# Optimization experiments

Measured on AMD Instinct MI355X. Metric: run time of the kernel, lower is better.

## Reference

```python
import jax, jax.numpy as jnp
import numpy as np
import math

# dims
B, T, D = 2, 1024, 1024
HQ, HKV, KD, VD = 16, 4, 64, 64   # query heads, kv heads, key dim, value dim
G = HQ // HKV                      # query group size
E, TOPK, CAP_FRAC, HID = 8, 2, 0.5, 2048
BASE = 10000.0
EPS = 1e-6


def setup_inputs() -> dict:
    key = jax.random.key(0)
    ks = jax.random.split(key, 12)
    s = jnp.float32(0.02)
    return {
        'x': jax.random.normal(ks[0], (B, T, D), jnp.float32),
        'wq': jax.random.normal(ks[1], (D, KD * HQ), jnp.float32) * s,
        'wk': jax.random.normal(ks[2], (D, KD * HKV), jnp.float32) * s,
        'wv': jax.random.normal(ks[3], (D, VD * HKV), jnp.float32) * s,
        'wo': jax.random.normal(ks[4], (G * HKV * VD, D), jnp.float32) * s,
        'router_w': jax.random.normal(ks[5], (D, E), jnp.float32) * s,
        'router_b': jax.random.normal(ks[6], (E,), jnp.float32) * s,
        'w1': jax.random.normal(ks[7], (E, D, HID), jnp.float32) * s,
        'w2': jax.random.normal(ks[8], (E, D, HID), jnp.float32) * s,
        'w3': jax.random.normal(ks[9], (E, HID, D), jnp.float32) * s,
        'norm1_scale': jnp.ones((D,), jnp.float32),
        'norm2_scale': jnp.ones((D,), jnp.float32),
    }


def _rms(x, scale):
    return x * jax.lax.rsqrt(jnp.mean(x * x, axis=-1, keepdims=True) + EPS) * scale


def _rope(x):
    # x: (B, t, H, d); rotary per RotaryEmbedding: tile(ticks,(1,2)), neg-half rotation
    t, d = x.shape[1], x.shape[3]
    thetas = BASE ** (-jnp.arange(0, d, 2, dtype=jnp.float32) / d)
    ticks = jnp.outer(jnp.arange(t, dtype=jnp.float32), thetas)
    ticks = jnp.tile(ticks, (1, 2))[None, :, None, :]
    cos, sin = jnp.cos(ticks).astype(x.dtype), jnp.sin(ticks).astype(x.dtype)
    x1, x2 = jnp.split(x, 2, axis=-1)
    neg = jnp.concatenate([-x2, x1], axis=-1)
    return x * cos + neg * sin


def reference(x, wq, wk, wv, wo, router_w, router_b, w1, w2, w3, norm1_scale, norm2_scale):
    b, t, d = x.shape
    # ---- pre-norm grouped-query attention with rotary, causal ----
    h = _rms(x, norm1_scale)
    q = (h @ wq).reshape(b, t, HQ, KD)
    k = (h @ wk).reshape(b, t, HKV, KD)
    v = (h @ wv).reshape(b, t, HKV, VD)
    q = _rope(q)
    k = _rope(k)
    qg = q.reshape(b, t, HKV, G, KD)
    scores = jnp.einsum('bthgk,bshk->bhgts', qg, k) / jnp.sqrt(jnp.asarray(KD, x.dtype))
    causal = jnp.tril(jnp.ones((t, t), bool))
    scores = jnp.where(causal, scores, jnp.asarray(-1e9, scores.dtype))
    probs = jax.nn.softmax(scores, axis=-1)
    attn = jnp.einsum('bhgts,bshv->bthgv', probs, v).reshape(b, t, HQ * VD)
    x = x + attn @ wo
    # ---- pre-norm top-k MoE feed-forward (capacity-masked dispatch/combine) ----
    h2 = _rms(x, norm2_scale)
    xf = h2.reshape(b * t, d)
    logits = xf.astype(jnp.float32) @ router_w + router_b        # router in fp32
    gate, assign = jax.lax.top_k(logits, TOPK)                   # (N,k)
    gate = jax.nn.softmax(gate, axis=-1).astype(x.dtype)
    cap = math.floor(b * t * CAP_FRAC)
    onehot = jax.nn.one_hot(assign, E, dtype=jnp.float32)        # (N,k,E)
    pos = jnp.cumsum(jnp.cumsum(onehot, axis=0), axis=1).astype(jnp.int32)
    mask = onehot * (pos < cap)                                  # capacity mask
    token_mask = jnp.sum(mask, axis=-1)                          # (N,k)
    choices = jnp.sum(jax.nn.one_hot(pos, cap, dtype=jnp.float32) * mask[..., None], axis=1)  # (N,E,cap)
    choices = choices.transpose(1, 2, 0)                         # (E,cap,N)
    exp_idx = jnp.einsum('tke,e->tk', mask, jnp.arange(E, dtype=jnp.float32)).astype(jnp.int32)
    pos_idx = jnp.einsum('tke,tke->tk', mask, pos.astype(jnp.float32)).astype(jnp.int32)
    grouped = jnp.einsum('ect,tD->ecD', choices.astype(x.dtype), xf)  # dispatch: (E,cap,D)
    # gated FF per expert: act(w2(x) * w1(x)) @ w3
    hh = jax.nn.gelu(jnp.einsum('ecd,edh->ech', grouped, w2) * jnp.einsum('ecd,edh->ech', grouped, w1))
    eout = jnp.einsum('ech,ehd->ecd', hh, w3)                    # (E,cap,D)
    gathered = eout[exp_idx, pos_idx].reshape(b, t, TOPK, d)
    tm = token_mask.reshape(b, t, TOPK)
    moe = jnp.where(tm[..., None] != 0, gathered, h2[:, :, None, :])  # dropped tokens fall back to input
    moe = jnp.einsum('btkD,btk->btD', moe, gate.reshape(b, t, TOPK))
    return x + moe
```

## Files before the change

### kernel.cpp

```cpp
#include <hip/hip_runtime.h>
#include <math.h>

#define Dm 1024
#define Tn 1024
#define Bn 2
#define NTOK 2048
#define HQn 16
#define HKVn 4
#define KDn 64
#define VDn 64
#define Gn 4
#define NE 8
#define CAPn 1024
#define HIDn 2048
#define QKVS 1536

using frag_ab = __attribute__((ext_vector_type(8))) short;
using f32x4  = __attribute__((ext_vector_type(4))) float;

__device__ __forceinline__ unsigned short f2bf(float f) {
    union { float f; unsigned int u; } v; v.f = f;
    unsigned int r = v.u + 0x7FFFu + ((v.u >> 16) & 1u);
    return (unsigned short)(r >> 16);
}
__device__ __forceinline__ float bf2f(unsigned short b) {
    union { unsigned int u; float f; } v; v.u = ((unsigned int)b) << 16;
    return v.f;
}
__device__ __forceinline__ float gelu_fast(float y) {
    float z = 0.7978845608028654f * (y + 0.044715f * y * y * y);
    float az = fabsf(z);
    float t = __expf(-2.f * az);
    float th = (1.f - t) / (1.f + t);
    th = copysignf(th, z);
    return 0.5f * y * (1.f + th);
}

#define GLOAD16(gp, lp) __builtin_amdgcn_global_load_lds( \
    (const __attribute__((address_space(1))) void*)(gp), \
    (__attribute__((address_space(3))) void*)(lp), 16, 0, 0)

#define LGKM_DRAIN() do { \
    asm volatile("s_waitcnt lgkmcnt(0)" ::: "memory"); \
    __builtin_amdgcn_sched_barrier(0); \
} while (0)

__global__ void rmsnorm_bf16_kernel(const float* __restrict__ x, const float* __restrict__ scale,
                                    unsigned short* __restrict__ out) {
    int row = blockIdx.x;
    const float* xr = x + (size_t)row * Dm;
    float ss = 0.f;
    for (int d = threadIdx.x; d < Dm; d += 256) { float v = xr[d]; ss += v * v; }
    __shared__ float red[256];
    red[threadIdx.x] = ss; __syncthreads();
    for (int s = 128; s > 0; s >>= 1) {
        if (threadIdx.x < s) red[threadIdx.x] += red[threadIdx.x + s];
        __syncthreads();
    }
    float inv = rsqrtf(red[0] * (1.f / Dm) + 1e-6f);
    for (int d = threadIdx.x; d < Dm; d += 256)
        out[(size_t)row * Dm + d] = f2bf(xr[d] * inv * scale[d]);
}

__global__ void rmsnorm_router_kernel(const float* __restrict__ x2, const float* __restrict__ scale,
                                      const float* __restrict__ rw, const float* __restrict__ rb,
                                      float* __restrict__ h2, int* __restrict__ assign,
                                      float* __restrict__ gate) {
    int row = blockIdx.x;
    const float* xr = x2 + (size_t)row * Dm;
    __shared__ float red[256];
    __shared__ float rowbuf[Dm];
    __shared__ float logits[NE];
    float v4[4]; float ss = 0.f;
    #pragma unroll
    for (int i = 0; i < 4; ++i) { v4[i] = xr[threadIdx.x + 256 * i]; ss += v4[i] * v4[i]; }
    red[threadIdx.x] = ss; __syncthreads();
    for (int s = 128; s > 0; s >>= 1) {
        if (threadIdx.x < s) red[threadIdx.x] += red[threadIdx.x + s];
        __syncthreads();
    }
    float inv = rsqrtf(red[0] * (1.f / Dm) + 1e-6f);
    #pragma unroll
    for (int i = 0; i < 4; ++i) {
        int d = threadIdx.x + 256 * i;
        float h = v4[i] * inv * scale[d];
        h2[(size_t)row * Dm + d] = h;
        rowbuf[d] = h;
    }
    __syncthreads();
    int e = threadIdx.x >> 5, lane32 = threadIdx.x & 31;
    float part = 0.f;
    for (int d = lane32; d < Dm; d += 32) part += rowbuf[d] * rw[(size_t)d * NE + e];
    for (int off = 16; off; off >>= 1) part += __shfl_down(part, off, 32);
    if (lane32 == 0) logits[e] = part + rb[e];
    __syncthreads();
    if (threadIdx.x == 0) {
        int i0 = 0; float m0 = logits[0];
        for (int i = 1; i < NE; ++i) if (logits[i] > m0) { m0 = logits[i]; i0 = i; }
        int i1 = -1; float m1 = -1e30f;
        for (int i = 0; i < NE; ++i) if (i != i0 && logits[i] > m1) { m1 = logits[i]; i1 = i; }
        float e1 = __expf(m1 - m0);
        float s = 1.f + e1;
        assign[row * 2] = i0; assign[row * 2 + 1] = i1;
        gate[row * 2] = 1.f / s; gate[row * 2 + 1] = e1 / s;
    }
}

__global__ void transpose_convert(const float* __restrict__ in, unsigned short* __restrict__ out,
                                  int R, int Cstride, int c_base) {
    int e = blockIdx.z;
    int Cext = gridDim.x * 64;
    in  += (size_t)e * R * Cstride;
    out += (size_t)e * R * Cext;
    __shared__ float T[64][65];
    int tid = threadIdx.x;
    int r0 = blockIdx.y * 64, c0 = blockIdx.x * 64;
    #pragma unroll
    for (int rep = 0; rep < 4; ++rep) {
        int r = (tid >> 4) + rep * 16;
        int c = (tid & 15) * 4;
        float4 v = *(const float4*)(in + (size_t)(r0 + r) * Cstride + c_base + c0 + c);
        T[r][c] = v.x; T[r][c + 1] = v.y; T[r][c + 2] = v.z; T[r][c + 3] = v.w;
    }
    __syncthreads();
    #pragma unroll
    for (int rep = 0; rep < 4; ++rep) {
        int c = rep * 16 + (tid >> 4);
        int r = (tid & 15) * 4;
        unsigned long long pk = (unsigned long long)f2bf(T[r][c])
                              | ((unsigned long long)f2bf(T[r + 1][c]) << 16)
                              | ((unsigned long long)f2bf(T[r + 2][c]) << 32)
                              | ((unsigned long long)f2bf(T[r + 3][c]) << 48);
        *(unsigned long long*)(out + (size_t)(c0 + c) * R + r0 + r) = pk;
    }
}

template<int MODE>
__global__ __launch_bounds__(256) void mfma_gemm2(const unsigned short* __restrict__ A,
                                                  const unsigned short* __restrict__ Bt,
                                                  void* __restrict__ Cout,
                                                  const float* __restrict__ R,
                                                  int N, int K, int nx) {
    int nwg = gridDim.x;
    int swz = (blockIdx.x & 7) * (nwg >> 3) + (blockIdx.x >> 3);
    int bx = swz % nx, by = swz / nx;
    int m0 = by * 128, n0 = bx * 128;
    __shared__ unsigned short As[3][128 * 32];
    __shared__ unsigned short Bs[3][128 * 32];
    int tid = threadIdx.x, wave = tid >> 6, lane = tid & 63;
    int quad = lane >> 4, r16 = lane & 15;
    int wm = wave & 1, wn = wave >> 1;
    int ch16 = ((lane & 3) ^ ((lane >> 3) & 3)) * 16;
    int rofs = (quad ^ ((r16 >> 1) & 3)) * 16;
    f32x4 acc[4][4];
    #pragma unroll
    for (int mt = 0; mt < 4; ++mt)
        #pragma unroll
        for (int nt = 0; nt < 4; ++nt) acc[mt][nt] = (f32x4){0.f, 0.f, 0.f, 0.f};
    const size_t rs = (size_t)K * 2;
    const char* ga0 = (const char*)A  + (size_t)m0 * rs;
    const char* gb0 = (const char*)Bt + (size_t)n0 * rs;
    auto stage = [&](int buf, int kk) {
        #pragma unroll
        for (int i = 0; i < 2; ++i) {
            int r = wave * 16 + i * 64 + (lane >> 2);
            size_t go = (size_t)r * rs + (size_t)kk * 2 + ch16;
            int lofs = wave * 1024 + i * 4096;
            GLOAD16(ga0 + go, (char*)As[buf] + lofs);
            GLOAD16(gb0 + go, (char*)Bs[buf] + lofs);
        }
    };
    int nsteps = K >> 5;
    stage(0, 0);
    if (nsteps > 1) stage(1, 32);
    int rd = 0, stg = 2;
    for (int t = 0; t < nsteps; ++t) {
        if (t) __builtin_amdgcn_s_barrier();
        if (t + 2 < nsteps) {
            stage(stg, (t + 2) << 5);
            stg = (stg == 2) ? 0 : stg + 1;
            asm volatile("s_waitcnt vmcnt(8)" ::: "memory");
        } else if (t + 1 < nsteps) {
            asm volatile("s_waitcnt vmcnt(4)" ::: "memory");
        } else {
            asm volatile("s_waitcnt vmcnt(0)" ::: "memory");
        }
        __builtin_amdgcn_s_barrier();
        asm volatile("" ::: "memory");
        const char* Ab = (const char*)As[rd];
        const char* Bb = (const char*)Bs[rd];
        rd = (rd == 2) ? 0 : rd + 1;
        frag_ab a[4], b[4];
        #pragma unroll
        for (int tt = 0; tt < 4; ++tt) {
            a[tt] = *(const frag_ab*)(Ab + (wm * 64 + tt * 16 + r16) * 64 + rofs);
            b[tt] = *(const frag_ab*)(Bb + (wn * 64 + tt * 16 + r16) * 64 + rofs);
        }
        #pragma unroll
        for (int mt = 0; mt < 4; ++mt)
            #pragma unroll
            for (int nt = 0; nt < 4; ++nt)
                acc[mt][nt] = __builtin_amdgcn_mfma_f32_16x16x32_bf16(a[mt], b[nt], acc[mt][nt], 0, 0, 0);
        LGKM_DRAIN();
    }
    #pragma unroll
    for (int mt = 0; mt < 4; ++mt)
        #pragma unroll
        for (int nt = 0; nt < 4; ++nt)
            #pragma unroll
            for (int r = 0; r < 4; ++r) {
                int m = m0 + wm * 64 + mt * 16 + quad * 4 + r;
                int n = n0 + wn * 64 + nt * 16 + r16;
                size_t idx = (size_t)m * N + n;
                float v = acc[mt][nt][r];
                if (MODE == 0) ((unsigned short*)Cout)[idx] = f2bf(v);
                else           ((float*)Cout)[idx] = v + R[idx];
            }
}

__global__ void rope_bf16(unsigned short* __restrict__ p) {
    int idx = blockIdx.x * 256 + threadIdx.x;
    const int QC = NTOK * HQn * 32;
    int i, col, row; float scale;
    if (idx < QC) {
        i = idx & 31; int h = (idx >> 5) & 15; row = idx >> 9;
        col = h * 64 + i; scale = 0.18033688011112042f;
    } else {
        int r = idx - QC;
        i = r & 31; int h = (r >> 5) & 3; row = r >> 7;
        col = 1024 + h * 64 + i; scale = 1.f;
    }
    int t = row & (Tn - 1);
    size_t base = (size_t)row * QKVS + col;
    float theta = __expf(-(float)i * (1.f / 32.f) * 9.210340371976184f);
    float ang = (float)t * theta;
    float c = cosf(ang), s = sinf(ang);
    float x1 = bf2f(p[base]), x2 = bf2f(p[base + 32]);
    p[base]      = f2bf((x1 * c - x2 * s) * scale);
    p[base + 32] = f2bf((x2 * c + x1 * s) * scale);
}

__global__ __launch_bounds__(256) void mfma_attn(const unsigned short* __restrict__ qkv,
                                                 unsigned short* __restrict__ attnb) {
    __shared__ unsigned short lds[24576];
    unsigned short* Ps = lds;
    unsigned short* Ks = lds + 8192;
    unsigned short* Vt = lds + 16384;
    int tid = threadIdx.x, wave = tid >> 6, lane = tid & 63;
    int quad = lane >> 4, r16 = lane & 15;
    int tq0 = blockIdx.x * 64, h = blockIdx.y, b = blockIdx.z;
    int kvh = h >> 2;
    const size_t rowb = QKVS * 2;

    {
        const char* qb = (const char*)(qkv + (size_t)(b * Tn + tq0) * QKVS + h * 64);
        int rloc = lane >> 3, ch = (lane & 7) ^ rloc;
        #pragma unroll
        for (int i = 0; i < 2; ++i) {
            int r0 = wave * 8 + i * 32;
            GLOAD16(qb + (size_t)(r0 + rloc) * rowb + ch * 16, (char*)Vt + r0 * 128);
        }
    }
    __syncthreads();
    frag_ab qf[2];
    #pragma unroll
    for (int ks = 0; ks < 2; ++ks) {
        int m = wave * 16 + r16;
        int ch = (ks * 4 + quad) ^ (m & 7);
        qf[ks] = *(const frag_ab*)((const char*)Vt + m * 128 + ch * 16);
    }

    float m_i[4], l_i[4];
    f32x4 O[4];
    #pragma unroll
    for (int r = 0; r < 4; ++r) { m_i[r] = -1e30f; l_i[r] = 0.f; }
    #pragma unroll
    for (int nt = 0; nt < 4; ++nt) O[nt] = (f32x4){0.f, 0.f, 0.f, 0.f};

    int nst = (blockIdx.x >> 1) + 1;
    int rel = (blockIdx.x & 1) * 64;
    for (int st = 0; st < nst; ++st) {
        int s0 = st * 128;
        __syncthreads();
        {
            const char* kb = (const char*)(qkv + (size_t)(b * Tn + s0) * QKVS + 1024 + kvh * 64);
            int rloc = lane >> 3, ch = (lane & 7) ^ rloc;
            #pragma unroll
            for (int i = 0; i < 4; ++i) {
                int r0 = wave * 8 + i * 32;
                GLOAD16(kb + (size_t)(r0 + rloc) * rowb + ch * 16, (char*)Ks + r0 * 128);
            }
        }
        {
            const unsigned short* vb = qkv + (size_t)(b * Tn + s0) * QKVS + 1280 + kvh * 64;
            int d4 = (tid & 15) * 4;
            #pragma unroll
            for (int pass = 0; pass < 4; ++pass) {
                int sl = 8 * wave + 2 * (lane >> 4) + pass * 32;
                ushort4 v0 = *(const ushort4*)(vb + (size_t)sl * QKVS + d4);
                ushort4 v1 = *(const ushort4*)(vb + (size_t)(sl + 1) * QKVS + d4);
                unsigned short a0[4] = {v0.x, v0.y, v0.z, v0.w};
                unsigned short a1[4] = {v1.x, v1.y, v1.z, v1.w};
                #pragma unroll
                for (int i = 0; i < 4; ++i) {
                    int d = d4 + i;
                    int col = (((sl >> 3) ^ (d & 15)) << 3) | (sl & 7);
                    *(unsigned int*)(Vt + d * 128 + col) =
                        (unsigned int)a0[i] | ((unsigned int)a1[i] << 16);
                }
            }
        }
        __syncthreads();
        f32x4 Sacc[8];
        #pragma unroll
        for (int nt = 0; nt < 8; ++nt) Sacc[nt] = (f32x4){0.f, 0.f, 0.f, 0.f};
        #pragma unroll
        for (int ks = 0; ks < 2; ++ks) {
            frag_ab kf[8];
            #pragma unroll
            for (int nt = 0; nt < 8; ++nt) {
                int n = nt * 16 + r16;
                int ch = (ks * 4 + quad) ^ (n & 7);
                kf[nt] = *(const frag_ab*)((const char*)Ks + n * 128 + ch * 16);
            }
            #pragma unroll
            for (int nt = 0; nt < 8; ++nt)
                Sacc[nt] = __builtin_amdgcn_mfma_f32_16x16x32_bf16(qf[ks], kf[nt], Sacc[nt], 0, 0, 0);
        }
        if (st == nst - 1) {
            int trow = wave * 16 + quad * 4 + rel;
            #pragma unroll
            for (int nt = 0; nt < 8; ++nt) {
                int scol = nt * 16 + r16;
                #pragma unroll
                for (int r = 0; r < 4; ++r)
                    if (scol > trow + r) Sacc[nt][r] = -1e30f;
            }
        }
        {
            float mx[4];
            #pragma unroll
            for (int r = 0; r < 4; ++r) {
                float m_ = Sacc[0][r];
                #pragma unroll
                for (int nt = 1; nt < 8; ++nt) m_ = fmaxf(m_, Sacc[nt][r]);
                mx[r] = m_;
            }
            #pragma unroll
            for (int off = 1; off < 16; off <<= 1)
                #pragma unroll
                for (int r = 0; r < 4; ++r) mx[r] = fmaxf(mx[r], __shfl_xor(mx[r], off));
            #pragma unroll
            for (int r = 0; r < 4; ++r) {
                float mn = fmaxf(m_i[r], mx[r]);
                float al = exp2f(m_i[r] - mn);
                m_i[r] = mn;
                l_i[r] *= al;
                #pragma unroll
                for (int nt = 0; nt < 4; ++nt) O[nt][r] *= al;
            }
            float rsum[4] = {0.f, 0.f, 0.f, 0.f};
            #pragma unroll
            for (int nt = 0; nt < 8; ++nt)
                #pragma unroll
                for (int r = 0; r < 4; ++r) {
                    float pv = exp2f(Sacc[nt][r] - m_i[r]);
                    Sacc[nt][r] = pv;
                    rsum[r] += pv;
                }
            #pragma unroll
            for (int off = 1; off < 16; off <<= 1)
                #pragma unroll
                for (int r = 0; r < 4; ++r) rsum[r] += __shfl_xor(rsum[r], off);
            #pragma unroll
            for (int r = 0; r < 4; ++r) l_i[r] += rsum[r];
            #pragma unroll
            for (int nt = 0; nt < 8; ++nt) {
                int scol = nt * 16 + r16;
                int chb = scol >> 3;
                #pragma unroll
                for (int r = 0; r < 4; ++r) {
                    int m = wave * 16 + quad * 4 + r;
                    int col = ((chb ^ (m & 15)) << 3) | (scol & 7);
                    Ps[m * 128 + col] = f2bf(Sacc[nt][r]);
                }
            }
        }
        #pragma unroll
        for (int ks = 0; ks < 4; ++ks) {
            frag_ab pa, vf[4];
            {
                int m = wave * 16 + r16;
                int ch = (ks * 4 + quad) ^ (m & 15);
                pa = *(const frag_ab*)((const char*)Ps + m * 256 + ch * 16);
            }
            #pragma unroll
            for (int nt = 0; nt < 4; ++nt) {
                int n = nt * 16 + r16;
                int ch = (ks * 4 + quad) ^ (n & 15);
                vf[nt] = *(const frag_ab*)((const char*)Vt + n * 256 + ch * 16);
            }
            #pragma unroll
            for (int nt = 0; nt < 4; ++nt)
                O[nt] = __builtin_amdgcn_mfma_f32_16x16x32_bf16(pa, vf[nt], O[nt], 0, 0, 0);
        }
    }
    {
        float inv[4];
        #pragma unroll
        for (int r = 0; r < 4; ++r) inv[r] = 1.f / l_i[r];
        #pragma unroll
        for (int nt = 0; nt < 4; ++nt)
            #pragma unroll
            for (int r = 0; r < 4; ++r) {
                int t = tq0 + wave * 16 + quad * 4 + r;
                int c = h * 64 + nt * 16 + r16;
                attnb[(size_t)(b * Tn + t) * Dm + c] = f2bf(O[nt][r] * inv[r]);
            }
    }
}

__global__ void scan_kernel(const int* __restrict__ assign, int* __restrict__ pos,
                            int* __restrict__ limit) {
    __shared__ int cnt[256][16];
    __shared__ int tot[16];
    int tid = threadIdx.x;
    int local[16];
    #pragma unroll
    for (int i = 0; i < 16; ++i) local[i] = 0;
    for (int r = 0; r < 8; ++r) {
        int t = tid * 8 + r;
        local[assign[t * 2]]++;
        local[8 + assign[t * 2 + 1]]++;
    }
    #pragma unroll
    for (int i = 0; i < 16; ++i) cnt[tid][i] = local[i];
    __syncthreads();
    if (tid < 16) {
        int run = 0;
        for (int th = 0; th < 256; ++th) { int v = cnt[th][tid]; cnt[th][tid] = run; run += v; }
        tot[tid] = run;
    }
    __syncthreads();
    int r0[NE], r1[NE];
    #pragma unroll
    for (int e = 0; e < NE; ++e) { r0[e] = cnt[tid][e]; r1[e] = cnt[tid][8 + e]; }
    for (int r = 0; r < 8; ++r) {
        int t = tid * 8 + r;
        int e0 = assign[t * 2], e1 = assign[t * 2 + 1];
        r0[e0]++; pos[t * 2] = r0[e0];
        r1[e1]++; pos[t * 2 + 1] = r0[e1] + r1[e1];
    }
    if (tid == 0)
        for (int e = 0; e < NE; ++e) {
            int C = tot[e] + tot[8 + e];
            limit[e] = C < (CAPn - 1) ? C : (CAPn - 1);
        }
}

__global__ void dispatch_kernel(const float* __restrict__ h2, const int* __restrict__ assign,
                                const int* __restrict__ pos, float* __restrict__ grouped) {
    int slot = blockIdx.x;
    int p = pos[slot];
    if (p >= CAPn) return;
    int e = assign[slot];
    const float* src = h2 + (size_t)(slot >> 1) * Dm;
    float* dst = grouped + ((size_t)e * CAPn + p) * Dm;
    for (int d = threadIdx.x; d < Dm; d += 256) atomicAdd(&dst[d], src[d]);
}

__global__ void convert_inplace(float* __restrict__ buf) {
    float* rp = buf + (size_t)blockIdx.x * Dm;
    float4 v = ((const float4*)rp)[threadIdx.x];
    __syncthreads();
    unsigned long long pk = (unsigned long long)f2bf(v.x)
                          | ((unsigned long long)f2bf(v.y) << 16)
                          | ((unsigned long long)f2bf(v.z) << 32)
                          | ((unsigned long long)f2bf(v.w) << 48);
    ((unsigned long long*)rp)[threadIdx.x] = pk;
}

__global__ __launch_bounds__(256) void mfma_gemm_fused(const float* __restrict__ grouped,
                                                       const unsigned short* __restrict__ B1t,
                                                       const unsigned short* __restrict__ B2t,
                                                       unsigned short* __restrict__ hh,
                                                       const int* __restrict__ limit) {
    int lin = blockIdx.x;
    int swz = (lin & 7) * (gridDim.x >> 3) + (lin >> 3);
    int e = swz >> 7;
    int m0 = ((swz >> 4) & 7) * 128;
    if (m0 > limit[e]) return;
    int n0 = (swz & 15) * 128;
    const char* ga0 = (const char*)grouped + ((size_t)e * CAPn + m0) * 4096;
    const unsigned short* b1 = B1t + (size_t)e * 1024 * Dm;
    const unsigned short* b2 = B2t + (size_t)e * 1024 * Dm;
    unsigned short* Ch = hh + (size_t)e * CAPn * 1024;
    __shared__ unsigned short As[3][128 * 32];
    __shared__ unsigned short Bs[3][128 * 32];
    int tid = threadIdx.x, wave = tid >> 6, lane = tid & 63;
    int quad = lane >> 4, r16 = lane & 15;
    int wm = wave & 1, wn = wave >> 1;
    int ch16 = ((lane & 3) ^ ((lane >> 3) & 3)) * 16;
    int rofs = (quad ^ ((r16 >> 1) & 3)) * 16;
    f32x4 acc[4][4];
    #pragma unroll
    for (int mt = 0; mt < 4; ++mt)
        #pragma unroll
        for (int nt = 0; nt < 4; ++nt) acc[mt][nt] = (f32x4){0.f, 0.f, 0.f, 0.f};
    auto stage = [&](int buf, int kk) {
        #pragma unroll
        for (int i = 0; i < 2; ++i) {
            int r = wave * 16 + i * 64 + (lane >> 2);
            int lofs = wave * 1024 + i * 4096;
            GLOAD16(ga0 + (size_t)r * 4096 + (size_t)kk * 2 + ch16, (char*)As[buf] + lofs);
            const unsigned short* bb = (r & 1) ? b2 : b1;
            size_t go = (size_t)((n0 + r) >> 1) * 2048 + (size_t)kk * 2 + ch16;
            GLOAD16((const char*)bb + go, (char*)Bs[buf] + lofs);
        }
    };
    const int nsteps = Dm >> 5;
    stage(0, 0);
    stage(1, 32);
    int rd = 0, stg = 2;
    for (int t = 0; t < nsteps; ++t) {
        if (t) __builtin_amdgcn_s_barrier();
        if (t + 2 < nsteps) {
            stage(stg, (t + 2) << 5);
            stg = (stg == 2) ? 0 : stg + 1;
            asm volatile("s_waitcnt vmcnt(8)" ::: "memory");
        } else if (t + 1 < nsteps) {
            asm volatile("s_waitcnt vmcnt(4)" ::: "memory");
        } else {
            asm volatile("s_waitcnt vmcnt(0)" ::: "memory");
        }
        __builtin_amdgcn_s_barrier();
        asm volatile("" ::: "memory");
        const char* Ab = (const char*)As[rd];
        const char* Bb = (const char*)Bs[rd];
        rd = (rd == 2) ? 0 : rd + 1;
        frag_ab a[4], b[4];
        #pragma unroll
        for (int tt = 0; tt < 4; ++tt) {
            a[tt] = *(const frag_ab*)(Ab + (wm * 64 + tt * 16 + r16) * 64 + rofs);
            b[tt] = *(const frag_ab*)(Bb + (wn * 64 + tt * 16 + r16) * 64 + rofs);
        }
        #pragma unroll
        for (int mt = 0; mt < 4; ++mt)
            #pragma unroll
            for (int nt = 0; nt < 4; ++nt)
                acc[mt][nt] = __builtin_amdgcn_mfma_f32_16x16x32_bf16(a[mt], b[nt], acc[mt][nt], 0, 0, 0);
        LGKM_DRAIN();
    }
    #pragma unroll
    for (int mt = 0; mt < 4; ++mt)
        #pragma unroll
        for (int nt = 0; nt < 4; ++nt)
            #pragma unroll
            for (int r = 0; r < 4; ++r) {
                float v = acc[mt][nt][r];
                float w = __shfl_xor(v, 1);
                if (!(r16 & 1)) {
                    int m = m0 + wm * 64 + mt * 16 + quad * 4 + r;
                    int j = (n0 + wn * 64 + nt * 16 + r16) >> 1;
                    Ch[(size_t)m * 1024 + j] = f2bf(gelu_fast(v * w));
                }
            }
}

__global__ __launch_bounds__(256) void mfma_gemm_w3(const unsigned short* __restrict__ hhA,
                                                    const unsigned short* __restrict__ hhB,
                                                    const unsigned short* __restrict__ Bt,
                                                    unsigned short* __restrict__ C,
                                                    const int* __restrict__ limit) {
    int lin = blockIdx.x;
    int swz = (lin & 7) * (gridDim.x >> 3) + (lin >> 3);
    int e = swz >> 7;
    int m0 = ((swz >> 4) & 7) * 128;
    if (m0 > limit[e]) return;
    int n0 = (swz & 15) * 64;
    const char* gaA = (const char*)hhA + ((size_t)e * CAPn + m0) * 2048;
    const char* gaB = (const char*)hhB + ((size_t)e * CAPn + m0) * 2048;
    const char* gb0 = (const char*)Bt + ((size_t)e * 1024 + n0) * 4096;
    C += (size_t)e * CAPn * 1024;
    __shared__ unsigned short As[3][128 * 32];
    __shared__ unsigned short Bs[3][64 * 32];
    int tid = threadIdx.x, wave = tid >> 6, lane = tid & 63;
    int quad = lane >> 4, r16 = lane & 15;
    int wm = wave & 1, wn = wave >> 1;
    int ch16 = ((lane & 3) ^ ((lane >> 3) & 3)) * 16;
    int rofs = (quad ^ ((r16 >> 1) & 3)) * 16;
    f32x4 acc[4][2];
    #pragma unroll
    for (int mt = 0; mt < 4; ++mt)
        #pragma unroll
        for (int nt = 0; nt < 2; ++nt) acc[mt][nt] = (f32x4){0.f, 0.f, 0.f, 0.f};
    auto stage = [&](int buf, int kk) {
        const char* ga = (kk < 1024) ? gaA : gaB;
        size_t kb = (size_t)(kk & 1023) * 2;
        #pragma unroll
        for (int i = 0; i < 2; ++i) {
            int r = wave * 16 + i * 64 + (lane >> 2);
            GLOAD16(ga + (size_t)r * 2048 + kb + ch16, (char*)As[buf] + wave * 1024 + i * 4096);
        }
        int r = wave * 16 + (lane >> 2);
        GLOAD16(gb0 + (size_t)r * 4096 + (size_t)kk * 2 + ch16, (char*)Bs[buf] + wave * 1024);
    };
    const int nsteps = HIDn >> 5;
    stage(0, 0);
    stage(1, 32);
    int rd = 0, stg = 2;
    for (int t = 0; t < nsteps; ++t) {
        if (t) __builtin_amdgcn_s_barrier();
        if (t + 2 < nsteps) {
            stage(stg, (t + 2) << 5);
            stg = (stg == 2) ? 0 : stg + 1;
            asm volatile("s_waitcnt vmcnt(6)" ::: "memory");
        } else if (t + 1 < nsteps) {
            asm volatile("s_waitcnt vmcnt(3)" ::: "memory");
        } else {
            asm volatile("s_waitcnt vmcnt(0)" ::: "memory");
        }
        __builtin_amdgcn_s_barrier();
        asm volatile("" ::: "memory");
        const char* Ab = (const char*)As[rd];
        const char* Bb = (const char*)Bs[rd];
        rd = (rd == 2) ? 0 : rd + 1;
        frag_ab a[4], b[2];
        #pragma unroll
        for (int tt = 0; tt < 4; ++tt)
            a[tt] = *(const frag_ab*)(Ab + (wm * 64 + tt * 16 + r16) * 64 + rofs);
        #pragma unroll
        for (int tt = 0; tt < 2; ++tt)
            b[tt] = *(const frag_ab*)(Bb + (wn * 32 + tt * 16 + r16) * 64 + rofs);
        #pragma unroll
        for (int mt = 0; mt < 4; ++mt)
            #pragma unroll
            for (int nt = 0; nt < 2; ++nt)
                acc[mt][nt] = __builtin_amdgcn_mfma_f32_16x16x32_bf16(a[mt], b[nt], acc[mt][nt], 0, 0, 0);
        LGKM_DRAIN();
    }
    #pragma unroll
    for (int mt = 0; mt < 4; ++mt)
        #pragma unroll
        for (int nt = 0; nt < 2; ++nt)
            #pragma unroll
            for (int r = 0; r < 4; ++r) {
                int m = m0 + wm * 64 + mt * 16 + quad * 4 + r;
                int n = n0 + wn * 32 + nt * 16 + r16;
                C[(size_t)m * 1024 + n] = f2bf(acc[mt][nt][r]);
            }
}

__global__ void combine_kernel(const float* __restrict__ x2, const float* __restrict__ h2,
                               const unsigned short* __restrict__ eout, const int* __restrict__ assign,
                               const int* __restrict__ pos, const float* __restrict__ gate,
                               float* __restrict__ out) {
    int t = blockIdx.x;
    int e0 = assign[t * 2], e1 = assign[t * 2 + 1];
    int p0 = pos[t * 2],   p1 = pos[t * 2 + 1];
    float g0 = gate[t * 2], g1 = gate[t * 2 + 1];
    bool k0 = p0 < CAPn, k1 = p1 < CAPn;
    const unsigned short* s0 = eout + ((size_t)e0 * CAPn + p0) * Dm;
    const unsigned short* s1 = eout + ((size_t)e1 * CAPn + p1) * Dm;
    const float* hb = h2 + (size_t)t * Dm;
    for (int d = threadIdx.x; d < Dm; d += 256) {
        float v0 = k0 ? bf2f(s0[d]) : hb[d];
        float v1 = k1 ? bf2f(s1[d]) : hb[d];
        out[(size_t)t * Dm + d] = x2[(size_t)t * Dm + d] + g0 * v0 + g1 * v1;
    }
}

extern "C" void kernel_launch(void* const* d_in, const int* in_sizes, int n_in,
                              void* d_out, int out_size, void* d_ws, size_t ws_size,
                              hipStream_t stream) {
    const float* x        = (const float*)d_in[0];
    const float* wq       = (const float*)d_in[1];
    const float* wk       = (const float*)d_in[2];
    const float* wv       = (const float*)d_in[3];
    const float* wo       = (const float*)d_in[4];
    const float* router_w = (const float*)d_in[5];
    const float* router_b = (const float*)d_in[6];
    const float* w1       = (const float*)d_in[7];
    const float* w2       = (const float*)d_in[8];
    const float* w3       = (const float*)d_in[9];
    const float* n1s      = (const float*)d_in[10];
    const float* n2s      = (const float*)d_in[11];
    float* out = (float*)d_out;
    unsigned char* ws = (unsigned char*)d_ws;
    const size_t MB = 1ull << 20;

    unsigned short* h_bf  = (unsigned short*)(ws + 0 * MB);
    unsigned short* qkv   = (unsigned short*)(ws + 4 * MB);
    unsigned short* wqkvt = (unsigned short*)(ws + 10 * MB);
    unsigned short* attnb = (unsigned short*)(ws + 13 * MB);
    unsigned short* wot   = (unsigned short*)(ws + 17 * MB);
    float* grouped_f32    = (float*)(ws + 0 * MB);
    unsigned short* eout  = (unsigned short*)(ws + 0 * MB);
    float* x2      = (float*)(ws + 32 * MB);
    float* h2      = (float*)(ws + 40 * MB);
    int*   assign  = (int*)  (ws + 48 * MB);
    int*   pos     = (int*)  (ws + 48 * MB + 65536);
    float* gate    = (float*)(ws + 48 * MB + 131072);
    int*   limit   = (int*)  (ws + 48 * MB + 196608);
    unsigned short* wtA = (unsigned short*)(ws + 49 * MB);
    unsigned short* wtB = (unsigned short*)(ws + 65 * MB);
    unsigned short* wt3 = (unsigned short*)(ws + 49 * MB);
    unsigned short* hhA = (unsigned short*)(ws + 81 * MB);
    unsigned short* hhB = (unsigned short*)(ws + 97 * MB);
    (void)in_sizes; (void)n_in; (void)out_size; (void)ws_size;

    transpose_convert<<<dim3(16, 16, 1), 256, 0, stream>>>(wq, wqkvt, Dm, Dm, 0);
    transpose_convert<<<dim3(4, 16, 1), 256, 0, stream>>>(wk, wqkvt + 1024 * 1024, Dm, 256, 0);
    transpose_convert<<<dim3(4, 16, 1), 256, 0, stream>>>(wv, wqkvt + 1280 * 1024, Dm, 256, 0);
    transpose_convert<<<dim3(16, 16, 1), 256, 0, stream>>>(wo, wot, Dm, Dm, 0);
    rmsnorm_bf16_kernel<<<NTOK, 256, 0, stream>>>(x, n1s, h_bf);
    mfma_gemm2<0><<<dim3((QKVS / 128) * (NTOK / 128)), 256, 0, stream>>>(h_bf, wqkvt, qkv, nullptr, QKVS, Dm, QKVS / 128);
    rope_bf16<<<(NTOK * (HQn + HKVn) * 32) / 256, 256, 0, stream>>>(qkv);
    mfma_attn<<<dim3(Tn / 64, HQn, Bn), 256, 0, stream>>>(qkv, attnb);
    mfma_gemm2<1><<<dim3((Dm / 128) * (NTOK / 128)), 256, 0, stream>>>(attnb, wot, x2, x, Dm, Dm, Dm / 128);
    rmsnorm_router_kernel<<<NTOK, 256, 0, stream>>>(x2, n2s, router_w, router_b, h2, assign, gate);
    scan_kernel<<<1, 256, 0, stream>>>(assign, pos, limit);
    hipMemsetAsync(grouped_f32, 0, (size_t)NE * CAPn * Dm * sizeof(float), stream);
    dispatch_kernel<<<NTOK * 2, 256, 0, stream>>>(h2, assign, pos, grouped_f32);
    convert_inplace<<<NE * CAPn, 256, 0, stream>>>(grouped_f32);
    transpose_convert<<<dim3(16, 16, NE), 256, 0, stream>>>(w1, wtA, Dm, HIDn, 0);
    transpose_convert<<<dim3(16, 16, NE), 256, 0, stream>>>(w2, wtB, Dm, HIDn, 0);
    mfma_gemm_fused<<<dim3(16 * (CAPn / 128) * NE), 256, 0, stream>>>(grouped_f32, wtA, wtB, hhA, limit);
    transpose_convert<<<dim3(16, 16, NE), 256, 0, stream>>>(w1, wtA, Dm, HIDn, 1024);
    transpose_convert<<<dim3(16, 16, NE), 256, 0, stream>>>(w2, wtB, Dm, HIDn, 1024);
    mfma_gemm_fused<<<dim3(16 * (CAPn / 128) * NE), 256, 0, stream>>>(grouped_f32, wtA, wtB, hhB, limit);
    transpose_convert<<<dim3(16, 32, NE), 256, 0, stream>>>(w3, wt3, HIDn, Dm, 0);
    mfma_gemm_w3<<<dim3(16 * (CAPn / 128) * NE), 256, 0, stream>>>(hhA, hhB, wt3, eout, limit);
    combine_kernel<<<NTOK, 256, 0, stream>>>(x2, h2, eout, assign, pos, gate, out);
}
```

Baseline: 537.8 us.

## Use BK=64 double-buffered GEMM tiles and fuse RoPE into QKV GEMM epilogue

All three MFMA GEMM kernels switch from a triple-buffered 32-wide K tile to a double-buffered 64-wide K tile, with a new XOR swizzle over 8 column groups. This halves the number of barrier-separated steps and runs two MFMA sub-steps per stage, at the cost of shallower prefetch and more LDS per block. Separately, rotary embedding and query scaling move into the QKV GEMM epilogue, which removes the standalone rope kernel and its read-modify-write pass over qkv. The fused epilogue rotates in fp32 before the single bf16 rounding, instead of rounding once before rope and again after.

Result: slower. 564.6 us (+5.0%).

```diff
diff --git a/kernel.cpp b/kernel.cpp
--- a/kernel.cpp
+++ b/kernel.cpp
@@ -145,13 +145,12 @@
     int swz = (blockIdx.x & 7) * (nwg >> 3) + (blockIdx.x >> 3);
     int bx = swz % nx, by = swz / nx;
     int m0 = by * 128, n0 = bx * 128;
-    __shared__ unsigned short As[3][128 * 32];
-    __shared__ unsigned short Bs[3][128 * 32];
-    int tid = threadIdx.x, wave = tid >> 6, lane = tid & 63;
+    __shared__ unsigned short As[2][128 * 64];
+    __shared__ unsigned short Bs[2][128 * 64];
+    int tid = threadIdx.x, lane = tid & 63;
+    int wave = tid >> 6;
     int quad = lane >> 4, r16 = lane & 15;
     int wm = wave & 1, wn = wave >> 1;
-    int ch16 = ((lane & 3) ^ ((lane >> 3) & 3)) * 16;
-    int rofs = (quad ^ ((r16 >> 1) & 3)) * 16;
     f32x4 acc[4][4];
     #pragma unroll
     for (int mt = 0; mt < 4; ++mt)
@@ -160,48 +159,72 @@
     const size_t rs = (size_t)K * 2;
     const char* ga0 = (const char*)A  + (size_t)m0 * rs;
     const char* gb0 = (const char*)Bt + (size_t)n0 * rs;
+    int srow8 = tid >> 3, scl = tid & 7;
     auto stage = [&](int buf, int kk) {
         #pragma unroll
-        for (int i = 0; i < 2; ++i) {
-            int r = wave * 16 + i * 64 + (lane >> 2);
-            size_t go = (size_t)r * rs + (size_t)kk * 2 + ch16;
-            int lofs = wave * 1024 + i * 4096;
+        for (int i = 0; i < 4; ++i) {
+            int row = i * 32 + srow8;
+            int cg = scl ^ (row & 7);
+            size_t go = (size_t)row * rs + (size_t)kk * 2 + cg * 16;
+            int lofs = row * 128 + scl * 16;
             GLOAD16(ga0 + go, (char*)As[buf] + lofs);
             GLOAD16(gb0 + go, (char*)Bs[buf] + lofs);
         }
     };
-    int nsteps = K >> 5;
+    int nsteps = K >> 6;
     stage(0, 0);
-    if (nsteps > 1) stage(1, 32);
-    int rd = 0, stg = 2;
     for (int t = 0; t < nsteps; ++t) {
         if (t) __builtin_amdgcn_s_barrier();
-        if (t + 2 < nsteps) {
-            stage(stg, (t + 2) << 5);
-            stg = (stg == 2) ? 0 : stg + 1;
+        if (t + 1 < nsteps) {
+            stage((t + 1) & 1, (t + 1) << 6);
             asm volatile("s_waitcnt vmcnt(8)" ::: "memory");
-        } else if (t + 1 < nsteps) {
-            asm volatile("s_waitcnt vmcnt(4)" ::: "memory");
         } else {
             asm volatile("s_waitcnt vmcnt(0)" ::: "memory");
         }
         __builtin_amdgcn_s_barrier();
         asm volatile("" ::: "memory");
-        const char* Ab = (const char*)As[rd];
-        const char* Bb = (const char*)Bs[rd];
-        rd = (rd == 2) ? 0 : rd + 1;
-        frag_ab a[4], b[4];
-        #pragma unroll
-        for (int tt = 0; tt < 4; ++tt) {
-            a[tt] = *(const frag_ab*)(Ab + (wm * 64 + tt * 16 + r16) * 64 + rofs);
-            b[tt] = *(const frag_ab*)(Bb + (wn * 64 + tt * 16 + r16) * 64 + rofs);
-        }
+        const char* Ab = (const char*)As[t & 1];
+        const char* Bb = (const char*)Bs[t & 1];
+        #pragma unroll
+        for (int ks = 0; ks < 2; ++ks) {
+            frag_ab a[4], b[4];
+            int cl = ((ks * 4 + quad) ^ (r16 & 7)) * 16;
+            #pragma unroll
+            for (int tt = 0; tt < 4; ++tt) {
+                a[tt] = *(const frag_ab*)(Ab + (wm * 64 + tt * 16 + r16) * 128 + cl);
+                b[tt] = *(const frag_ab*)(Bb + (wn * 64 + tt * 16 + r16) * 128 + cl);
+            }
+            #pragma unroll
+            for (int mt = 0; mt < 4; ++mt)
+                #pragma unroll
+                for (int nt = 0; nt < 4; ++nt)
+                    acc[mt][nt] = __builtin_amdgcn_mfma_f32_16x16x32_bf16(a[mt], b[nt], acc[mt][nt], 0, 0, 0);
+        }
+        LGKM_DRAIN();
+    }
+    if (MODE == 0 && n0 < 1280) {
+        float qs = (n0 < 1024) ? 0.18033688011112042f : 1.f;
+        float th0 = __expf(-(float)(r16)      * (1.f / 32.f) * 9.210340371976184f);
+        float th1 = __expf(-(float)(r16 + 16) * (1.f / 32.f) * 9.210340371976184f);
         #pragma unroll
         for (int mt = 0; mt < 4; ++mt)
             #pragma unroll
-            for (int nt = 0; nt < 4; ++nt)
-                acc[mt][nt] = __builtin_amdgcn_mfma_f32_16x16x32_bf16(a[mt], b[nt], acc[mt][nt], 0, 0, 0);
-        LGKM_DRAIN();
+            for (int r = 0; r < 4; ++r) {
+                int m = m0 + wm * 64 + mt * 16 + quad * 4 + r;
+                float tf = (float)(m & (Tn - 1));
+                {
+                    float ang = tf * th0; float c = cosf(ang), s = sinf(ang);
+                    float x1 = acc[mt][0][r], x2 = acc[mt][2][r];
+                    acc[mt][0][r] = (x1 * c - x2 * s) * qs;
+                    acc[mt][2][r] = (x2 * c + x1 * s) * qs;
+                }
+                {
+                    float ang = tf * th1; float c = cosf(ang), s = sinf(ang);
+                    float x1 = acc[mt][1][r], x2 = acc[mt][3][r];
+                    acc[mt][1][r] = (x1 * c - x2 * s) * qs;
+                    acc[mt][3][r] = (x2 * c + x1 * s) * qs;
+                }
+            }
     }
     #pragma unroll
     for (int mt = 0; mt < 4; ++mt)
@@ -216,28 +239,6 @@
                 if (MODE == 0) ((unsigned short*)Cout)[idx] = f2bf(v);
                 else           ((float*)Cout)[idx] = v + R[idx];
             }
-}
-
-__global__ void rope_bf16(unsigned short* __restrict__ p) {
-    int idx = blockIdx.x * 256 + threadIdx.x;
-    const int QC = NTOK * HQn * 32;
-    int i, col, row; float scale;
-    if (idx < QC) {
-        i = idx & 31; int h = (idx >> 5) & 15; row = idx >> 9;
-        col = h * 64 + i; scale = 0.18033688011112042f;
-    } else {
-        int r = idx - QC;
-        i = r & 31; int h = (r >> 5) & 3; row = r >> 7;
-        col = 1024 + h * 64 + i; scale = 1.f;
-    }
-    int t = row & (Tn - 1);
-    size_t base = (size_t)row * QKVS + col;
-    float theta = __expf(-(float)i * (1.f / 32.f) * 9.210340371976184f);
-    float ang = (float)t * theta;
-    float c = cosf(ang), s = sinf(ang);
-    float x1 = bf2f(p[base]), x2 = bf2f(p[base + 32]);
-    p[base]      = f2bf((x1 * c - x2 * s) * scale);
-    p[base + 32] = f2bf((x2 * c + x1 * s) * scale);
 }
 
 __global__ __launch_bounds__(256) void mfma_attn(const unsigned short* __restrict__ qkv,
@@ -495,60 +496,59 @@
     const unsigned short* b1 = B1t + (size_t)e * 1024 * Dm;
     const unsigned short* b2 = B2t + (size_t)e * 1024 * Dm;
     unsigned short* Ch = hh + (size_t)e * CAPn * 1024;
-    __shared__ unsigned short As[3][128 * 32];
-    __shared__ unsigned short Bs[3][128 * 32];
-    int tid = threadIdx.x, wave = tid >> 6, lane = tid & 63;
+    __shared__ unsigned short As[2][128 * 64];
+    __shared__ unsigned short Bs[2][128 * 64];
+    int tid = threadIdx.x, lane = tid & 63;
+    int wave = tid >> 6;
     int quad = lane >> 4, r16 = lane & 15;
     int wm = wave & 1, wn = wave >> 1;
-    int ch16 = ((lane & 3) ^ ((lane >> 3) & 3)) * 16;
-    int rofs = (quad ^ ((r16 >> 1) & 3)) * 16;
     f32x4 acc[4][4];
     #pragma unroll
     for (int mt = 0; mt < 4; ++mt)
         #pragma unroll
         for (int nt = 0; nt < 4; ++nt) acc[mt][nt] = (f32x4){0.f, 0.f, 0.f, 0.f};
+    int srow8 = tid >> 3, scl = tid & 7;
     auto stage = [&](int buf, int kk) {
         #pragma unroll
-        for (int i = 0; i < 2; ++i) {
-            int r = wave * 16 + i * 64 + (lane >> 2);
-            int lofs = wave * 1024 + i * 4096;
-            GLOAD16(ga0 + (size_t)r * 4096 + (size_t)kk * 2 + ch16, (char*)As[buf] + lofs);
-            const unsigned short* bb = (r & 1) ? b2 : b1;
-            size_t go = (size_t)((n0 + r) >> 1) * 2048 + (size_t)kk * 2 + ch16;
+        for (int i = 0; i < 4; ++i) {
+            int row = i * 32 + srow8;
+            int cg = scl ^ (row & 7);
+            int lofs = row * 128 + scl * 16;
+            GLOAD16(ga0 + (size_t)row * 4096 + (size_t)kk * 2 + cg * 16, (char*)As[buf] + lofs);
+            const unsigned short* bb = (row & 1) ? b2 : b1;
+            size_t go = (size_t)((n0 + row) >> 1) * 2048 + (size_t)kk * 2 + cg * 16;
             GLOAD16((const char*)bb + go, (char*)Bs[buf] + lofs);
         }
     };
-    const int nsteps = Dm >> 5;
+    const int nsteps = Dm >> 6;
     stage(0, 0);
-    stage(1, 32);
-    int rd = 0, stg = 2;
     for (int t = 0; t < nsteps; ++t) {
         if (t) __builtin_amdgcn_s_barrier();
-        if (t + 2 < nsteps) {
-            stage(stg, (t + 2) << 5);
-            stg = (stg == 2) ? 0 : stg + 1;
+        if (t + 1 < nsteps) {
+            stage((t + 1) & 1, (t + 1) << 6);
             asm volatile("s_waitcnt vmcnt(8)" ::: "memory");
-        } else if (t + 1 < nsteps) {
-            asm volatile("s_waitcnt vmcnt(4)" ::: "memory");
         } else {
             asm volatile("s_waitcnt vmcnt(0)" ::: "memory");
         }
         __builtin_amdgcn_s_barrier();
         asm volatile("" ::: "memory");
-        const char* Ab = (const char*)As[rd];
-        const char* Bb = (const char*)Bs[rd];
-        rd = (rd == 2) ? 0 : rd + 1;
-        frag_ab a[4], b[4];
-        #pragma unroll
-        for (int tt = 0; tt < 4; ++tt) {
-            a[tt] = *(const frag_ab*)(Ab + (wm * 64 + tt * 16 + r16) * 64 + rofs);
-            b[tt] = *(const frag_ab*)(Bb + (wn * 64 + tt * 16 + r16) * 64 + rofs);
-        }
-        #pragma unroll
-        for (int mt = 0; mt < 4; ++mt)
-            #pragma unroll
-            for (int nt = 0; nt < 4; ++nt)
-                acc[mt][nt] = __builtin_amdgcn_mfma_f32_16x16x32_bf16(a[mt], b[nt], acc[mt][nt], 0, 0, 0);
+        const char* Ab = (const char*)As[t & 1];
+        const char* Bb = (const char*)Bs[t & 1];
+        #pragma unroll
+        for (int ks = 0; ks < 2; ++ks) {
+            frag_ab a[4], b[4];
+            int cl = ((ks * 4 + quad) ^ (r16 & 7)) * 16;
+            #pragma unroll
+            for (int tt = 0; tt < 4; ++tt) {
+                a[tt] = *(const frag_ab*)(Ab + (wm * 64 + tt * 16 + r16) * 128 + cl);
+                b[tt] = *(const frag_ab*)(Bb + (wn * 64 + tt * 16 + r16) * 128 + cl);
+            }
+            #pragma unroll
+            for (int mt = 0; mt < 4; ++mt)
+                #pragma unroll
+                for (int nt = 0; nt < 4; ++nt)
+                    acc[mt][nt] = __builtin_amdgcn_mfma_f32_16x16x32_bf16(a[mt], b[nt], acc[mt][nt], 0, 0, 0);
+        }
         LGKM_DRAIN();
     }
     #pragma unroll
@@ -582,61 +582,66 @@
     const char* gaB = (const char*)hhB + ((size_t)e * CAPn + m0) * 2048;
     const char* gb0 = (const char*)Bt + ((size_t)e * 1024 + n0) * 4096;
     C += (size_t)e * CAPn * 1024;
-    __shared__ unsigned short As[3][128 * 32];
-    __shared__ unsigned short Bs[3][64 * 32];
-    int tid = threadIdx.x, wave = tid >> 6, lane = tid & 63;
+    __shared__ unsigned short As[2][128 * 64];
+    __shared__ unsigned short Bs[2][64 * 64];
+    int tid = threadIdx.x, lane = tid & 63;
+    int wave = tid >> 6;
     int quad = lane >> 4, r16 = lane & 15;
     int wm = wave & 1, wn = wave >> 1;
-    int ch16 = ((lane & 3) ^ ((lane >> 3) & 3)) * 16;
-    int rofs = (quad ^ ((r16 >> 1) & 3)) * 16;
     f32x4 acc[4][2];
     #pragma unroll
     for (int mt = 0; mt < 4; ++mt)
         #pragma unroll
         for (int nt = 0; nt < 2; ++nt) acc[mt][nt] = (f32x4){0.f, 0.f, 0.f, 0.f};
+    int srow8 = tid >> 3, scl = tid & 7;
     auto stage = [&](int buf, int kk) {
         const char* ga = (kk < 1024) ? gaA : gaB;
         size_t kb = (size_t)(kk & 1023) * 2;
         #pragma unroll
+        for (int i = 0; i < 4; ++i) {
+            int row = i * 32 + srow8;
+            int cg = scl ^ (row & 7);
+            GLOAD16(ga + (size_t)row * 2048 + kb + cg * 16,
+                    (char*)As[buf] + row * 128 + scl * 16);
+        }
+        #pragma unroll
         for (int i = 0; i < 2; ++i) {
-            int r = wave * 16 + i * 64 + (lane >> 2);
-            GLOAD16(ga + (size_t)r * 2048 + kb + ch16, (char*)As[buf] + wave * 1024 + i * 4096);
-        }
-        int r = wave * 16 + (lane >> 2);
-        GLOAD16(gb0 + (size_t)r * 4096 + (size_t)kk * 2 + ch16, (char*)Bs[buf] + wave * 1024);
+            int row = i * 32 + srow8;
+            int cg = scl ^ (row & 7);
+            GLOAD16(gb0 + (size_t)row * 4096 + (size_t)kk * 2 + cg * 16,
+                    (char*)Bs[buf] + row * 128 + scl * 16);
+        }
     };
-    const int nsteps = HIDn >> 5;
+    const int nsteps = HIDn >> 6;
     stage(0, 0);
-    stage(1, 32);
-    int rd = 0, stg = 2;
     for (int t = 0; t < nsteps; ++t) {
         if (t) __builtin_amdgcn_s_barrier();
-        if (t + 2 < nsteps) {
-            stage(stg, (t + 2) << 5);
-            stg = (stg == 2) ? 0 : stg + 1;
+        if (t + 1 < nsteps) {
+            stage((t + 1) & 1, (t + 1) << 6);
             asm volatile("s_waitcnt vmcnt(6)" ::: "memory");
-        } else if (t + 1 < nsteps) {
-            asm volatile("s_waitcnt vmcnt(3)" ::: "memory");
         } else {
             asm volatile("s_waitcnt vmcnt(0)" ::: "memory");
         }
         __builtin_amdgcn_s_barrier();
         asm volatile("" ::: "memory");
-        const char* Ab = (const char*)As[rd];
-        const char* Bb = (const char*)Bs[rd];
-        rd = (rd == 2) ? 0 : rd + 1;
-        frag_ab a[4], b[2];
-        #pragma unroll
-        for (int tt = 0; tt < 4; ++tt)
-            a[tt] = *(const frag_ab*)(Ab + (wm * 64 + tt * 16 + r16) * 64 + rofs);
-        #pragma unroll
-        for (int tt = 0; tt < 2; ++tt)
-            b[tt] = *(const frag_ab*)(Bb + (wn * 32 + tt * 16 + r16) * 64 + rofs);
-        #pragma unroll
-        for (int mt = 0; mt < 4; ++mt)
-            #pragma unroll
-            for (int nt = 0; nt < 2; ++nt)
-                acc[mt][nt] = __builtin_amdgcn_mfma_f32_16x16x32_bf16(a[mt], b[nt], acc[mt][nt], 0, 0, 0);
+        const char* Ab = (const char*)As[t & 1];
+        const char* Bb = (const char*)Bs[t & 1];
+        #pragma unroll
+        for (int ks = 0; ks < 2; ++ks) {
+            frag_ab a[4], b[2];
+            int cl = ((ks * 4 + quad) ^ (r16 & 7)) * 16;
+            #pragma unroll
+            for (int tt = 0; tt < 4; ++tt)
+                a[tt] = *(const frag_ab*)(Ab + (wm * 64 + tt * 16 + r16) * 128 + cl);
+            #pragma unroll
+            for (int tt = 0; tt < 2; ++tt)
+                b[tt] = *(const frag_ab*)(Bb + (wn * 32 + tt * 16 + r16) * 128 + cl);
+            #pragma unroll
+            for (int mt = 0; mt < 4; ++mt)
+                #pragma unroll
+                for (int nt = 0; nt < 2; ++nt)
+                    acc[mt][nt] = __builtin_amdgcn_mfma_f32_16x16x32_bf16(a[mt], b[nt], acc[mt][nt], 0, 0, 0);
+        }
         LGKM_DRAIN();
     }
     #pragma unroll
@@ -715,7 +720,6 @@
     transpose_convert<<<dim3(16, 16, 1), 256, 0, stream>>>(wo, wot, Dm, Dm, 0);
     rmsnorm_bf16_kernel<<<NTOK, 256, 0, stream>>>(x, n1s, h_bf);
     mfma_gemm2<0><<<dim3((QKVS / 128) * (NTOK / 128)), 256, 0, stream>>>(h_bf, wqkvt, qkv, nullptr, QKVS, Dm, QKVS / 128);
-    rope_bf16<<<(NTOK * (HQn + HKVn) * 32) / 256, 256, 0, stream>>>(qkv);
     mfma_attn<<<dim3(Tn / 64, HQn, Bn), 256, 0, stream>>>(qkv, attnb);
     mfma_gemm2<1><<<dim3((Dm / 128) * (NTOK / 128)), 256, 0, stream>>>(attnb, wot, x2, x, Dm, Dm, Dm / 128);
     rmsnorm_router_kernel<<<NTOK, 256, 0, stream>>>(x2, n2s, router_w, router_b, h2, assign, gate);
```
